# Optimization experiments

Measured on AMD Instinct MI355X. Metric: run time of the kernel, lower is better.

The kernel has to match this reference:

```python
import jax, jax.numpy as jnp
import numpy as np

B, IN_DIM, N, L = 8, 2, 512, 64
D_MODEL = 32
D_FF = 32          # must equal D_MODEL: output_bn is BatchNorm2d(d_model) applied to skip
DEPTH = 3          # blocks=3 * layers=1; dilation resets to 1 each block -> all dilations = 1
KS = 2             # temporal kernel size
EPS = 1e-5         # BatchNorm eps


def setup_inputs() -> dict:
    key = jax.random.key(0)
    ks = jax.random.split(key, 16)
    s = 0.1  # weight scale for numeric sanity
    x = jax.random.normal(ks[0], (B, IN_DIM, N, L), jnp.float32)
    a = jax.random.uniform(ks[1], (N, N), jnp.float32)
    adj = a / a.sum(axis=1, keepdims=True)  # row-stochastic diffusion matrix
    return {
        "x": x,
        "adj": adj,
        "Wstart": jax.random.normal(ks[2], (D_MODEL, IN_DIM), jnp.float32) * s,
        "bstart": jnp.zeros((D_MODEL,), jnp.float32),
        "Wf": jax.random.normal(ks[3], (DEPTH, D_MODEL, D_MODEL, KS), jnp.float32) * s,
        "bf": jnp.zeros((DEPTH, D_MODEL), jnp.float32),
        "Wg": jax.random.normal(ks[4], (DEPTH, D_MODEL, D_MODEL, KS), jnp.float32) * s,
        "bg": jnp.zeros((DEPTH, D_MODEL), jnp.float32),
        "Wskip": jax.random.normal(ks[5], (DEPTH, D_FF, D_MODEL), jnp.float32) * s,
        "bskip": jnp.zeros((DEPTH, D_FF), jnp.float32),
        "Wgc": jax.random.normal(ks[6], (DEPTH, D_MODEL, 3 * D_MODEL), jnp.float32) * s,
        "bgc": jnp.zeros((DEPTH, D_MODEL), jnp.float32),
        "gcbn_g": jnp.ones((DEPTH, D_MODEL), jnp.float32),
        "gcbn_b": jnp.zeros((DEPTH, D_MODEL), jnp.float32),
        "bn_g": jnp.ones((DEPTH, D_MODEL), jnp.float32),
        "bn_b": jnp.zeros((DEPTH, D_MODEL), jnp.float32),
        "obn_g": jnp.ones((D_MODEL,), jnp.float32),
        "obn_b": jnp.zeros((D_MODEL,), jnp.float32),
    }


def _c1x1(x, W, b):
    # Conv2d with (1,1) kernel == channel mixing. x: [b,c,n,l], W: [o,c]
    return jnp.einsum('bcnl,oc->bonl', x, W) + b[None, :, None, None]


def _dconv(x, W, b, d):
    # Conv2d kernel (1,2), dilation d along time (valid). W: [o,c,2]
    Lx = x.shape[-1]
    y = (jnp.einsum('bcnl,oc->bonl', x[..., :Lx - d], W[..., 0])
         + jnp.einsum('bcnl,oc->bonl', x[..., d:], W[..., 1]))
    return y + b[None, :, None, None]


def _bn(x, g, bta):
    # eval-mode BatchNorm2d: running_mean=0, running_var=1
    inv = g / jnp.sqrt(1.0 + EPS)
    return x * inv[None, :, None, None] + bta[None, :, None, None]


def reference(x, adj, Wstart, bstart, Wf, bf, Wg, bg, Wskip, bskip,
              Wgc, bgc, gcbn_g, gcbn_b, bn_g, bn_b, obn_g, obn_b):
    rf = 1 + DEPTH * (KS - 1)  # receptive field with dilation 1 per layer
    h = _c1x1(x, Wstart, bstart)
    if h.shape[-1] < rf:
        h = jnp.pad(h, ((0, 0), (0, 0), (0, 0), (rf - h.shape[-1], 0)))
    skip = None
    for i in range(DEPTH):
        residual = h
        filt = jnp.tanh(_dconv(h, Wf[i], bf[i], 1))
        gate = jax.nn.sigmoid(_dconv(h, Wg[i], bg[i], 1))
        h = filt * gate
        s = _c1x1(h, Wskip[i], bskip[i])
        skip = s if skip is None else s + skip[..., -s.shape[-1]:]
        if i == DEPTH - 1:
            break
        # order-2 graph diffusion: h, A h, A^2 h -> concat -> 1x1 conv -> BN (dropout: eval noop)
        x1 = jnp.einsum('bcnl,nm->bcml', h, adj)
        x2 = jnp.einsum('bcnl,nm->bcml', x1, adj)
        cat = jnp.concatenate([h, x1, x2], axis=1)
        g = _bn(_c1x1(cat, Wgc[i], bgc[i]), gcbn_g[i], gcbn_b[i])
        h = g + residual[..., -g.shape[-1]:]
        h = _bn(h, bn_g[i], bn_b[i])
    out = _bn(skip, obn_g, obn_b)
    return jnp.swapaxes(out, 1, 3)  # [B, L', N, C]
```

## Files before the change

### kernel.cpp

```cpp
#include <hip/hip_runtime.h>
#include <hip/hip_bf16.h>

#define B_     8
#define CIN_   2
#define N_     512
#define C_     32
#define L_     64
#define LOUT_  61
#define BUF_   ((size_t)(8*32*512*64))

typedef __hip_bfloat16 bf16;
typedef unsigned short ushort_t;
typedef unsigned int u32;
typedef __attribute__((ext_vector_type(8))) unsigned short us8;
typedef __attribute__((ext_vector_type(8))) short bf16x8;
typedef __attribute__((ext_vector_type(4))) float f32x4;

static __device__ __forceinline__ float bits2f(ushort_t u) {
    return __uint_as_float(((unsigned)u) << 16);
}
static __device__ __forceinline__ ushort_t f2bits(float v) {
    unsigned u = __float_as_uint(v);
    return (ushort_t)((u + 0x7fffu + ((u >> 16) & 1u)) >> 16);
}

static __device__ __forceinline__ void gload16(const ushort_t* g, ushort_t* l) {
    __builtin_amdgcn_global_load_lds(
        (const __attribute__((address_space(1))) unsigned int*)g,
        (__attribute__((address_space(3))) unsigned int*)l,
        16, 0, 0);
}

static __device__ __forceinline__ u32 swap1(u32 v) {
    return (u32)__builtin_amdgcn_update_dpp(0, (int)v, 0xB1, 0xF, 0xF, true);
}

__global__ void k_start(const float* __restrict__ x,
                        const float* __restrict__ Wst,
                        const float* __restrict__ bst,
                        ushort_t* __restrict__ h) {
    int idx = blockIdx.x * 256 + threadIdx.x;
    int l0 = (idx & 7) * 8;
    int n  = (idx >> 3) & 511;
    int o  = (idx >> 12) & 31;
    int b  = idx >> 17;
    float w0 = Wst[o * 2], w1 = Wst[o * 2 + 1], bb = bst[o];
    int xbase = (b * CIN_ * N_ + n) * L_ + l0;
    float va[8], vb[8];
    *(float4*)&va[0] = *(const float4*)(x + xbase);
    *(float4*)&va[4] = *(const float4*)(x + xbase + 4);
    *(float4*)&vb[0] = *(const float4*)(x + xbase + N_ * L_);
    *(float4*)&vb[4] = *(const float4*)(x + xbase + N_ * L_ + 4);
    us8 r;
    #pragma unroll
    for (int k = 0; k < 8; ++k) r[k] = f2bits(bb + va[k] * w0 + vb[k] * w1);
    *(us8*)(h + (size_t)idx * 8) = r;
}

__global__ void k_transA(const float* __restrict__ adj, ushort_t* __restrict__ adjT) {
    __shared__ float buf[64][65];
    int ti = blockIdx.x & 7;
    int tj = blockIdx.x >> 3;
    int t = threadIdx.x;
    for (int r = 0; r < 16; ++r) {
        int e = t + 256 * r;
        int rl = e >> 6, cl = e & 63;
        buf[rl][cl] = adj[(size_t)(ti * 64 + rl) * 512 + tj * 64 + cl];
    }
    __syncthreads();
    for (int r = 0; r < 16; ++r) {
        int e = t + 256 * r;
        int ml = e >> 6, nl = e & 63;
        adjT[(size_t)(tj * 64 + ml) * 512 + ti * 64 + nl] = f2bits(buf[nl][ml]);
    }
}

__global__ __launch_bounds__(256, 2) void k_sq(const ushort_t* __restrict__ adjT,
                                               ushort_t* __restrict__ adj2T) {
    __shared__ __align__(16) ushort_t lds2[8192];
    ushort_t* As = lds2;
    ushort_t* Bs = lds2 + 4096;
    int mt = blockIdx.x & 7, nc = blockIdx.x >> 3;
    int t = threadIdx.x, lane = t & 63, w = t >> 6;
    int la = lane & 15, q = lane >> 4;
    f32x4 acc[4];
    #pragma unroll
    for (int mi = 0; mi < 4; ++mi) acc[mi] = (f32x4)0.f;
    for (int p0 = 0; p0 < 512; p0 += 64) {
        __syncthreads();
        #pragma unroll
        for (int r = 0; r < 2; ++r) {
            int e = t + 256 * r, ml = e >> 3, oct = e & 7;
            int sw = ((oct + (ml >> 3)) & 7) << 3;
            *(us8*)(As + ml * 64 + sw) =
                *(const us8*)(adjT + (size_t)(mt * 64 + ml) * 512 + p0 + oct * 8);
            *(us8*)(Bs + ml * 64 + sw) =
                *(const us8*)(adjT + (size_t)(p0 + ml) * 512 + nc * 64 + oct * 8);
        }
        __syncthreads();
        #pragma unroll
        for (int ks = 0; ks < 2; ++ks) {
            bf16x8 a[4];
            #pragma unroll
            for (int mi = 0; mi < 4; ++mi) {
                int m = mi * 16 + la;
                int bl = (ks * 4 + q + (m >> 3)) & 7;
                a[mi] = *(const bf16x8*)(As + m * 64 + bl * 8);
            }
            bf16x8 bv;
            {
                int n = w * 16 + la;
                int rot = ((n >> 3) + ks * 4 + q) & 7;
                int col = rot * 8 + (n & 7);
                const ushort_t* p = Bs + (ks * 32 + q * 8) * 64 + col;
                #pragma unroll
                for (int j = 0; j < 8; ++j) bv[j] = (short)p[j * 64];
            }
            #pragma unroll
            for (int mi = 0; mi < 4; ++mi)
                acc[mi] = __builtin_amdgcn_mfma_f32_16x16x32_bf16(a[mi], bv, acc[mi], 0, 0, 0);
        }
    }
    __syncthreads();
    ushort_t* Ys = lds2;
    #pragma unroll
    for (int mi = 0; mi < 4; ++mi)
        #pragma unroll
        for (int r = 0; r < 4; ++r)
            Ys[(mi * 16 + q * 4 + r) * 72 + w * 16 + la] = f2bits(acc[mi][r]);
    __syncthreads();
    #pragma unroll
    for (int r = 0; r < 2; ++r) {
        int e = t + 256 * r, ml = e >> 3, oct = e & 7;
        us8 v = *(const us8*)(Ys + ml * 72 + oct * 8);
        *(us8*)(adj2T + (size_t)(mt * 64 + ml) * 512 + nc * 64 + oct * 8) = v;
    }
}

__global__ __launch_bounds__(256, 6) void k_gs_mfma(
        const ushort_t* __restrict__ h,
        const float* __restrict__ Wf, const float* __restrict__ bfp,
        const float* __restrict__ Wg, const float* __restrict__ bgp,
        const float* __restrict__ Wsk, const float* __restrict__ bsk,
        ushort_t* __restrict__ G, float* __restrict__ out,
        int off, int mode, int storeG,
        const float* __restrict__ og, const float* __restrict__ obb) {
    __shared__ __align__(16) ushort_t lds[10496];
    ushort_t* Hs  = lds;
    ushort_t* Asf = lds + 4608;
    ushort_t* Asg = lds + 6912;
    ushort_t* As2 = lds + 9216;
    __shared__ float bfv[32], bgv[32], bsv[32];
    int t = threadIdx.x;
    int b = blockIdx.x >> 8, n0 = (blockIdx.x & 255) * 2;
    int lane = t & 63, w = t >> 6;
    int ng = w & 1, cg = w >> 1;
    int la = lane & 15, q = lane >> 4;

    {
        int o = t >> 3, k8 = (t & 7) * 8;
        us8 vf, vg;
        #pragma unroll
        for (int i = 0; i < 8; ++i) {
            int k = k8 + i, c = k & 31, tap = k >> 5;
            vf[i] = f2bits(Wf[o * 64 + c * 2 + tap]);
            vg[i] = f2bits(Wg[o * 64 + c * 2 + tap]);
        }
        *(us8*)(Asf + o * 72 + k8) = vf;
        *(us8*)(Asg + o * 72 + k8) = vg;
        if (k8 < 32) {
            us8 vs;
            #pragma unroll
            for (int i = 0; i < 8; ++i) vs[i] = f2bits(Wsk[o * 32 + k8 + i]);
            *(us8*)(As2 + o * 40 + k8) = vs;
        }
        if (t < 32) { bfv[t] = bfp[t]; bgv[t] = bgp[t]; bsv[t] = bsk[t]; }
    }
    const ushort_t* hb = h + (size_t)(b * 32) * 512 * 64;
    #pragma unroll
    for (int r = 0; r < 2; ++r) {
        int e = t + 256 * r;
        int row = e >> 3, oct = e & 7;
        us8 v = *(const us8*)(hb + ((size_t)(row >> 1) * 512 + n0 + (row & 1)) * 64 + oct * 8);
        int sw = (oct + row + (row >> 5)) & 7;
        *(us8*)(Hs + row * 72 + sw * 8) = v;
    }
    if (t < 128) {
        int row = t >> 1, hf = t & 1;
        *(uint2*)(Hs + row * 72 + 64 + hf * 4) = make_uint2(0u, 0u);
    }
    __syncthreads();

    bf16x8 af[2][2], ag[2][2];
    #pragma unroll
    for (int mt = 0; mt < 2; ++mt)
        #pragma unroll
        for (int ks = 0; ks < 2; ++ks) {
            af[mt][ks] = *(const bf16x8*)(Asf + (mt * 16 + la) * 72 + ks * 32 + q * 8);
            ag[mt][ks] = *(const bf16x8*)(Asg + (mt * 16 + la) * 72 + ks * 32 + q * 8);
        }

    f32x4 fa[2][2], ga[2][2];
    #pragma unroll
    for (int mt = 0; mt < 2; ++mt)
        #pragma unroll
        for (int cl = 0; cl < 2; ++cl) { fa[mt][cl] = (f32x4)0.f; ga[mt][cl] = (f32x4)0.f; }
    #pragma unroll
    for (int cl = 0; cl < 2; ++cl) {
        int ct = cg * 2 + cl;
        #pragma unroll
        for (int ks = 0; ks < 2; ++ks) {
            int le = ct * 16 + la + ks;
            bf16x8 bv;
            #pragma unroll
            for (int j = 0; j < 8; ++j) {
                int row = (q * 8 + j) * 2 + ng;
                int pos = (le < 64) ? ((((le >> 3) + row + (row >> 5)) & 7) * 8 + (le & 7)) : le;
                bv[j] = (short)Hs[row * 72 + pos];
            }
            #pragma unroll
            for (int mt = 0; mt < 2; ++mt) {
                fa[mt][cl] = __builtin_amdgcn_mfma_f32_16x16x32_bf16(af[mt][ks], bv, fa[mt][cl], 0, 0, 0);
                ga[mt][cl] = __builtin_amdgcn_mfma_f32_16x16x32_bf16(ag[mt][ks], bv, ga[mt][cl], 0, 0, 0);
            }
        }
    }
    __syncthreads();

    #pragma unroll
    for (int mt = 0; mt < 2; ++mt)
        #pragma unroll
        for (int cl = 0; cl < 2; ++cl)
            #pragma unroll
            for (int r = 0; r < 4; ++r) {
                int o = mt * 16 + q * 4 + r;
                float fv = fa[mt][cl][r] + bfv[o];
                float gv = ga[mt][cl][r] + bgv[o];
                float ef = __expf(2.f * fv);
                float act = (1.f - 2.f / (ef + 1.f)) * (1.f / (1.f + __expf(-gv)));
                int l = (cg * 2 + cl) * 16 + la;
                int row = o * 2 + ng;
                int sw = ((l >> 3) + row + (row >> 5)) & 7;
                Hs[row * 72 + sw * 8 + (l & 7)] = f2bits(act);
            }
    __syncthreads();

    bf16x8 a2[2];
    a2[0] = *(const bf16x8*)(As2 + la * 40 + q * 8);
    a2[1] = *(const bf16x8*)(As2 + (16 + la) * 40 + q * 8);
    f32x4 sa[2][2];
    #pragma unroll
    for (int mt = 0; mt < 2; ++mt)
        #pragma unroll
        for (int cl = 0; cl < 2; ++cl) sa[mt][cl] = (f32x4)0.f;
    #pragma unroll
    for (int cl = 0; cl < 2; ++cl) {
        int le = (cg * 2 + cl) * 16 + la + off;
        bf16x8 bv;
        #pragma unroll
        for (int j = 0; j < 8; ++j) {
            int row = (q * 8 + j) * 2 + ng;
            int pos = (le < 64) ? ((((le >> 3) + row + (row >> 5)) & 7) * 8 + (le & 7)) : le;
            bv[j] = (short)Hs[row * 72 + pos];
        }
        sa[0][cl] = __builtin_amdgcn_mfma_f32_16x16x32_bf16(a2[0], bv, sa[0][cl], 0, 0, 0);
        sa[1][cl] = __builtin_amdgcn_mfma_f32_16x16x32_bf16(a2[1], bv, sa[1][cl], 0, 0, 0);
    }
    __syncthreads();

    if (storeG) {
        #pragma unroll
        for (int r = 0; r < 2; ++r) {
            int e = t + 256 * r;
            int row = e >> 3, oct = e & 7;
            int sw = (oct + row + (row >> 5)) & 7;
            us8 v = *(const us8*)(Hs + row * 72 + sw * 8);
            *(us8*)(G + ((size_t)(b * 32 + (row >> 1)) * 512 + n0 + (row & 1)) * 64 + oct * 8) = v;
        }
    }
    __syncthreads();

    float* St = (float*)lds;
    const float rbn = rsqrtf(1.f + 1e-5f);
    #pragma unroll
    for (int mt = 0; mt < 2; ++mt)
        #pragma unroll
        for (int cl = 0; cl < 2; ++cl) {
            int col = ng * 64 + (cg * 2 + cl) * 16 + la;
            int ob = mt * 16 + q * 4;
            float4 sv = make_float4(sa[mt][cl][0] + bsv[ob],
                                    sa[mt][cl][1] + bsv[ob + 1],
                                    sa[mt][cl][2] + bsv[ob + 2],
                                    sa[mt][cl][3] + bsv[ob + 3]);
            *(float4*)(St + col * 36 + ob) = sv;
        }
    __syncthreads();
    {
        int col = t >> 1, o0 = (t & 1) * 16;
        int nr = col >> 6, l = col & 63;
        if (l < LOUT_) {
            float* po = out + ((size_t)(b * LOUT_ + l) * 512 + n0 + nr) * 32 + o0;
            #pragma unroll
            for (int i = 0; i < 4; ++i) {
                float4 s = *(float4*)(St + col * 36 + o0 + i * 4);
                if (mode == 0) {
                    *(float4*)(po + i * 4) = s;
                } else {
                    float4 old = *(float4*)(po + i * 4);
                    float4 vv = make_float4(old.x + s.x, old.y + s.y,
                                            old.z + s.z, old.w + s.w);
                    if (mode == 2) {
                        int ob = o0 + i * 4;
                        vv.x = vv.x * (og[ob] * rbn) + obb[ob];
                        vv.y = vv.y * (og[ob + 1] * rbn) + obb[ob + 1];
                        vv.z = vv.z * (og[ob + 2] * rbn) + obb[ob + 2];
                        vv.w = vv.w * (og[ob + 3] * rbn) + obb[ob + 3];
                    }
                    *(float4*)(po + i * 4) = vv;
                }
            }
        }
    }
}

__global__ __launch_bounds__(256, 2) void k_diffuse2(
        const ushort_t* __restrict__ X, const ushort_t* __restrict__ adjT,
        const ushort_t* __restrict__ adj2T,
        ushort_t* __restrict__ Y1, ushort_t* __restrict__ Y2) {
    __shared__ __align__(16) ushort_t lds[32768];
    int cp = blockIdx.x & 15;
    int mt = (blockIdx.x >> 4) & 7;
    int b  = blockIdx.x >> 7;
    int t  = threadIdx.x;
    int lane = t & 63, w = t >> 6;
    int c_loc = w & 1, lh = w >> 1;
    int m0 = mt * 64;
    int la = lane & 15, q = lane >> 4;
    int p_ = la & 1;
    u32 sel = p_ ? 0x07060302u : 0x05040100u;
    const ushort_t* Xb = X + (size_t)(b * 32 + cp * 2) * 512 * 64;
    f32x4 acc1[4][2], acc2[4][2];
    #pragma unroll
    for (int mi = 0; mi < 4; ++mi)
        #pragma unroll
        for (int li = 0; li < 2; ++li) { acc1[mi][li] = (f32x4)0.f; acc2[mi][li] = (f32x4)0.f; }

    union U { u32 u[4]; bf16x8 v; };

    auto STAGE = [&](int n0, ushort_t* bb) {
        ushort_t* As1b = bb;
        ushort_t* As2b = bb + 4096;
        ushort_t* Xsb  = bb + 8192;
        #pragma unroll
        for (int r = 0; r < 2; ++r) {
            int e = t + 256 * r, ml = e >> 3, s = e & 7;
            int og = ((s - (ml >> 3)) & 7) * 8;
            gload16(adjT  + (size_t)(m0 + ml) * 512 + n0 + og, As1b + (size_t)e * 8);
            gload16(adj2T + (size_t)(m0 + ml) * 512 + n0 + og, As2b + (size_t)e * 8);
        }
        #pragma unroll
        for (int r = 0; r < 4; ++r) {
            int e = t + 256 * r;
            int cl = e >> 9, nl = (e >> 3) & 63, s = e & 7;
            int og = ((s - nl - (nl >> 3)) & 7) * 8;
            gload16(Xb + ((size_t)cl * 512 + n0 + nl) * 64 + og, Xsb + (size_t)e * 8);
        }
    };

    STAGE(0, lds);
    __syncthreads();

    for (int it = 0; it < 8; ++it) {
        ushort_t* cur = lds + (it & 1) * 16384;
        if (it < 7) STAGE((it + 1) * 64, lds + ((it + 1) & 1) * 16384);
        ushort_t* As1 = cur;
        ushort_t* As2 = cur + 4096;
        ushort_t* Xs  = cur + 8192;
        const ushort_t* xc = Xs + c_loc * 4096;
        #pragma unroll
        for (int ks = 0; ks < 2; ++ks) {
            bf16x8 a1[4], a2v[4];
            #pragma unroll
            for (int mi = 0; mi < 4; ++mi) {
                int m = mi * 16 + la;
                int bl = (ks * 4 + q + (m >> 3)) & 7;
                a1[mi]  = *(const bf16x8*)(As1 + m * 64 + bl * 8);
                a2v[mi] = *(const bf16x8*)(As2 + m * 64 + bl * 8);
            }
            bf16x8 bb[2];
            #pragma unroll
            for (int li = 0; li < 2; ++li) {
                int l2 = lh * 32 + li * 16 + (la & ~1);
                int r0 = ks * 32 + q * 8 + p_ * 4;
                int brot = ((l2 >> 3) + p_ * 4 + ks * 4 + q) & 7;
                u32 o0 = *(const u32*)(xc + (r0 + 0) * 64 + (((brot + 0) & 7) << 3) + (l2 & 7));
                u32 o1 = *(const u32*)(xc + (r0 + 1) * 64 + (((brot + 1) & 7) << 3) + (l2 & 7));
                u32 o2 = *(const u32*)(xc + (r0 + 2) * 64 + (((brot + 2) & 7) << 3) + (l2 & 7));
                u32 o3 = *(const u32*)(xc + (r0 + 3) * 64 + (((brot + 3) & 7) << 3) + (l2 & 7));
                u32 s0 = swap1(o0), s1 = swap1(o1), s2 = swap1(o2), s3 = swap1(o3);
                u32 lo0 = p_ ? s0 : o0, lo1 = p_ ? s1 : o1;
                u32 lo2 = p_ ? s2 : o2, lo3 = p_ ? s3 : o3;
                u32 hi0 = p_ ? o0 : s0, hi1 = p_ ? o1 : s1;
                u32 hi2 = p_ ? o2 : s2, hi3 = p_ ? o3 : s3;
                U u;
                u.u[0] = __builtin_amdgcn_perm(lo1, lo0, sel);
                u.u[1] = __builtin_amdgcn_perm(lo3, lo2, sel);
                u.u[2] = __builtin_amdgcn_perm(hi1, hi0, sel);
                u.u[3] = __builtin_amdgcn_perm(hi3, hi2, sel);
                bb[li] = u.v;
            }
            #pragma unroll
            for (int mi = 0; mi < 4; ++mi)
                #pragma unroll
                for (int li = 0; li < 2; ++li) {
                    acc1[mi][li] = __builtin_amdgcn_mfma_f32_16x16x32_bf16(a1[mi],  bb[li], acc1[mi][li], 0, 0, 0);
                    acc2[mi][li] = __builtin_amdgcn_mfma_f32_16x16x32_bf16(a2v[mi], bb[li], acc2[mi][li], 0, 0, 0);
                }
        }
        __syncthreads();
    }

    ushort_t* Ys = lds;
    #pragma unroll
    for (int pass = 0; pass < 2; ++pass) {
        __syncthreads();
        f32x4 (*src)[2] = pass ? acc2 : acc1;
        #pragma unroll
        for (int mi = 0; mi < 4; ++mi)
            #pragma unroll
            for (int li = 0; li < 2; ++li)
                #pragma unroll
                for (int r = 0; r < 4; ++r) {
                    int row = mi * 16 + q * 4 + r;
                    int col = lh * 32 + li * 16 + la;
                    Ys[c_loc * 4608 + row * 72 + col] = f2bits(src[mi][li][r]);
                }
        __syncthreads();
        ushort_t* Yo = pass ? Y2 : Y1;
        int c = t >> 7, mrem = t & 127;
        int m = mrem >> 1, lq = mrem & 1;
        #pragma unroll
        for (int r = 0; r < 4; ++r) {
            int l0 = lq * 32 + r * 8;
            us8 v = *(const us8*)(Ys + c * 4608 + m * 72 + l0);
            *(us8*)(Yo + ((size_t)(b * 32 + cp * 2 + c) * 512 + m0 + m) * 64 + l0) = v;
        }
    }
}

__global__ __launch_bounds__(256, 2) void k_gc3_mfma(
        ushort_t* __restrict__ G, const ushort_t* __restrict__ X1,
        const ushort_t* __restrict__ X2, const ushort_t* __restrict__ hres,
        const float* __restrict__ Wgc, const float* __restrict__ bgc,
        const float* __restrict__ gg, const float* __restrict__ gb,
        const float* __restrict__ bg2, const float* __restrict__ bb2) {
    __shared__ __align__(16) ushort_t cat[384 * 72];
    __shared__ __align__(16) ushort_t hr[128 * 64];
    __shared__ __align__(16) ushort_t Aw[32 * 104];
    __shared__ float prm[5][32];
    int t = threadIdx.x;
    int b = blockIdx.x >> 7, n0 = (blockIdx.x & 127) * 4;
    int lane = t & 63, w = t >> 6;
    int la = lane & 15, q = lane >> 4;

    #pragma unroll
    for (int r = 0; r < 12; ++r) {
        int e = t + 256 * r;
        int row = e >> 3, oct = e & 7;
        int k = row >> 2;
        const ushort_t* src = (k < 32) ? G : ((k < 64) ? X1 : X2);
        us8 v = *(const us8*)(src + ((size_t)(b * 32 + (k & 31)) * 512 + n0 + (row & 3)) * 64 + oct * 8);
        int sw = (oct + row + (row >> 5)) & 7;
        *(us8*)(cat + row * 72 + sw * 8) = v;
    }
    #pragma unroll
    for (int r = 0; r < 4; ++r) {
        int e = t + 256 * r;
        int row = e >> 3, oct = e & 7;
        us8 v = *(const us8*)(hres + ((size_t)(b * 32 + (row >> 2)) * 512 + n0 + (row & 3)) * 64 + oct * 8);
        *(us8*)(hr + row * 64 + oct * 8) = v;
    }
    for (int e = t; e < 384; e += 256) {
        int o = e / 12, oct = e % 12;
        us8 v;
        #pragma unroll
        for (int i = 0; i < 8; ++i) v[i] = f2bits(Wgc[o * 96 + oct * 8 + i]);
        *(us8*)(Aw + o * 104 + oct * 8) = v;
    }
    if (t < 32) {
        prm[0][t] = bgc[t]; prm[1][t] = gg[t]; prm[2][t] = gb[t];
        prm[3][t] = bg2[t]; prm[4][t] = bb2[t];
    }
    __syncthreads();

    bf16x8 a[2][3];
    #pragma unroll
    for (int mt = 0; mt < 2; ++mt)
        #pragma unroll
        for (int ks = 0; ks < 3; ++ks)
            a[mt][ks] = *(const bf16x8*)(Aw + (mt * 16 + la) * 104 + ks * 32 + q * 8);

    f32x4 acc[2][4];
    #pragma unroll
    for (int mt = 0; mt < 2; ++mt)
        #pragma unroll
        for (int ct = 0; ct < 4; ++ct) acc[mt][ct] = (f32x4)0.f;
    #pragma unroll
    for (int ct = 0; ct < 4; ++ct) {
        int le = ct * 16 + la;
        #pragma unroll
        for (int ks = 0; ks < 3; ++ks) {
            bf16x8 bv;
            #pragma unroll
            for (int j = 0; j < 8; ++j) {
                int row = (ks * 32 + q * 8 + j) * 4 + w;
                int sw = ((le >> 3) + row + (row >> 5)) & 7;
                bv[j] = (short)cat[row * 72 + sw * 8 + (le & 7)];
            }
            acc[0][ct] = __builtin_amdgcn_mfma_f32_16x16x32_bf16(a[0][ks], bv, acc[0][ct], 0, 0, 0);
            acc[1][ct] = __builtin_amdgcn_mfma_f32_16x16x32_bf16(a[1][ks], bv, acc[1][ct], 0, 0, 0);
        }
    }
    __syncthreads();

    const float rbn = rsqrtf(1.f + 1e-5f);
    #pragma unroll
    for (int mt = 0; mt < 2; ++mt)
        #pragma unroll
        for (int ct = 0; ct < 4; ++ct)
            #pragma unroll
            for (int r = 0; r < 4; ++r) {
                int o = mt * 16 + q * 4 + r;
                int l = ct * 16 + la;
                float v = acc[mt][ct][r] + prm[0][o];
                v = v * (prm[1][o] * rbn) + prm[2][o];
                float res = (l < 63) ? bits2f(hr[(o * 4 + w) * 64 + l + 1]) : 0.f;
                v = (v + res) * (prm[3][o] * rbn) + prm[4][o];
                int row = o * 4 + w;
                int sw = ((l >> 3) + row + (row >> 5)) & 7;
                cat[row * 72 + sw * 8 + (l & 7)] = f2bits(v);
            }
    __syncthreads();
    #pragma unroll
    for (int r = 0; r < 4; ++r) {
        int e = t + 256 * r;
        int row = e >> 3, oct = e & 7;
        int sw = (oct + row + (row >> 5)) & 7;
        us8 v = *(const us8*)(cat + row * 72 + sw * 8);
        *(us8*)(G + ((size_t)(b * 32 + (row >> 2)) * 512 + n0 + (row & 3)) * 64 + oct * 8) = v;
    }
}

extern "C" void kernel_launch(void* const* d_in, const int* in_sizes, int n_in,
                              void* d_out, int out_size, void* d_ws, size_t ws_size,
                              hipStream_t stream) {
    const float* x      = (const float*)d_in[0];
    const float* adj    = (const float*)d_in[1];
    const float* Wstart = (const float*)d_in[2];
    const float* bstart = (const float*)d_in[3];
    const float* Wf     = (const float*)d_in[4];
    const float* bf_    = (const float*)d_in[5];
    const float* Wg     = (const float*)d_in[6];
    const float* bg     = (const float*)d_in[7];
    const float* Wskip  = (const float*)d_in[8];
    const float* bskip  = (const float*)d_in[9];
    const float* Wgc    = (const float*)d_in[10];
    const float* bgc    = (const float*)d_in[11];
    const float* gcbn_g = (const float*)d_in[12];
    const float* gcbn_b = (const float*)d_in[13];
    const float* bn_g   = (const float*)d_in[14];
    const float* bn_b   = (const float*)d_in[15];
    const float* obn_g  = (const float*)d_in[16];
    const float* obn_b  = (const float*)d_in[17];
    float* out = (float*)d_out;

    ushort_t* P0    = (ushort_t*)d_ws;
    ushort_t* P1    = P0 + BUF_;
    ushort_t* P2    = P1 + BUF_;
    ushort_t* P3    = P2 + BUF_;
    ushort_t* adjT  = P3 + BUF_;
    ushort_t* adj2T = adjT + 512 * 512;

    k_transA<<<64, 256, 0, stream>>>(adj, adjT);
    k_sq<<<64, 256, 0, stream>>>(adjT, adj2T);
    k_start<<<4096, 256, 0, stream>>>(x, Wstart, bstart, P0);

    ushort_t* h  = P0;
    ushort_t* Gb = P1;
    for (int i = 0; i < 3; ++i) {
        int mode = (i == 0) ? 0 : ((i == 2) ? 2 : 1);
        k_gs_mfma<<<2048, 256, 0, stream>>>(h, Wf + i * 2048, bf_ + i * 32,
                                            Wg + i * 2048, bg + i * 32,
                                            Wskip + i * 1024, bskip + i * 32,
                                            Gb, out, 2 - i, mode, (i < 2) ? 1 : 0,
                                            obn_g, obn_b);
        if (i == 2) break;
        k_diffuse2<<<1024, 256, 0, stream>>>(Gb, adjT, adj2T, P2, P3);
        k_gc3_mfma<<<1024, 256, 0, stream>>>(Gb, P2, P3, h,
                                             Wgc + i * 3072, bgc + i * 32,
                                             gcbn_g + i * 32, gcbn_b + i * 32,
                                             bn_g + i * 32, bn_b + i * 32);
        ushort_t* tmp = h; h = Gb; Gb = tmp;
    }
}
```

Before: 320.7 us.

## Halve gc3 tile to 2 nodes per block and pack B-operand reads

The graph-conv mixing kernel now handles 2 nodes per block instead of 4 and launches twice as many blocks. Its LDS footprint shrinks, the rotated layout drops padding, and the tile is loaded with async gload16 copies. B fragments are built from 32-bit LDS reads combined with byte-perm instructions, replacing per-element 16-bit loads. Launch bounds change for both the gate/skip kernel (fewer waves) and the gc3 kernel (more waves). The swizzle and perm logic is intricate and could introduce layout errors.

New measurement: 306.3 us. 4.5% less time.

```diff
diff --git a/kernel.cpp b/kernel.cpp
--- a/kernel.cpp
+++ b/kernel.cpp
@@ -137,7 +137,7 @@
     }
 }
 
-__global__ __launch_bounds__(256, 6) void k_gs_mfma(
+__global__ __launch_bounds__(256, 4) void k_gs_mfma(
         const ushort_t* __restrict__ h,
         const float* __restrict__ Wf, const float* __restrict__ bfp,
         const float* __restrict__ Wg, const float* __restrict__ bgp,
@@ -448,37 +448,41 @@
     }
 }
 
-__global__ __launch_bounds__(256, 2) void k_gc3_mfma(
+__global__ __launch_bounds__(256, 4) void k_gc3_mfma(
         ushort_t* __restrict__ G, const ushort_t* __restrict__ X1,
         const ushort_t* __restrict__ X2, const ushort_t* __restrict__ hres,
         const float* __restrict__ Wgc, const float* __restrict__ bgc,
         const float* __restrict__ gg, const float* __restrict__ gb,
         const float* __restrict__ bg2, const float* __restrict__ bb2) {
-    __shared__ __align__(16) ushort_t cat[384 * 72];
-    __shared__ __align__(16) ushort_t hr[128 * 64];
+    __shared__ __align__(16) ushort_t cat[192 * 64];
+    __shared__ __align__(16) ushort_t hr[64 * 64];
     __shared__ __align__(16) ushort_t Aw[32 * 104];
     __shared__ float prm[5][32];
     int t = threadIdx.x;
-    int b = blockIdx.x >> 7, n0 = (blockIdx.x & 127) * 4;
+    int b = blockIdx.x >> 8, n0 = (blockIdx.x & 255) * 2;
     int lane = t & 63, w = t >> 6;
+    int ng = w & 1, cg = w >> 1;
     int la = lane & 15, q = lane >> 4;
-
-    #pragma unroll
-    for (int r = 0; r < 12; ++r) {
+    int p_ = la & 1;
+    u32 sel = p_ ? 0x07060302u : 0x05040100u;
+
+    #pragma unroll
+    for (int r = 0; r < 6; ++r) {
+        int e = t + 256 * r;
+        int row = e >> 3, s = e & 7;
+        int k = row >> 1, nr = row & 1;
+        int rot = k + (k >> 3);
+        int og = ((s - rot) & 7) * 8;
+        const ushort_t* src = (k < 32) ? G : ((k < 64) ? X1 : X2);
+        gload16(src + ((size_t)(b * 32 + (k & 31)) * 512 + n0 + nr) * 64 + og,
+                cat + (size_t)e * 8);
+    }
+    #pragma unroll
+    for (int r = 0; r < 2; ++r) {
         int e = t + 256 * r;
         int row = e >> 3, oct = e & 7;
-        int k = row >> 2;
-        const ushort_t* src = (k < 32) ? G : ((k < 64) ? X1 : X2);
-        us8 v = *(const us8*)(src + ((size_t)(b * 32 + (k & 31)) * 512 + n0 + (row & 3)) * 64 + oct * 8);
-        int sw = (oct + row + (row >> 5)) & 7;
-        *(us8*)(cat + row * 72 + sw * 8) = v;
-    }
-    #pragma unroll
-    for (int r = 0; r < 4; ++r) {
-        int e = t + 256 * r;
-        int row = e >> 3, oct = e & 7;
-        us8 v = *(const us8*)(hres + ((size_t)(b * 32 + (row >> 2)) * 512 + n0 + (row & 3)) * 64 + oct * 8);
-        *(us8*)(hr + row * 64 + oct * 8) = v;
+        gload16(hres + ((size_t)(b * 32 + (row >> 1)) * 512 + n0 + (row & 1)) * 64 + oct * 8,
+                hr + (size_t)e * 8);
     }
     for (int e = t; e < 384; e += 256) {
         int o = e / 12, oct = e % 12;
@@ -500,25 +504,35 @@
         for (int ks = 0; ks < 3; ++ks)
             a[mt][ks] = *(const bf16x8*)(Aw + (mt * 16 + la) * 104 + ks * 32 + q * 8);
 
-    f32x4 acc[2][4];
-    #pragma unroll
-    for (int mt = 0; mt < 2; ++mt)
-        #pragma unroll
-        for (int ct = 0; ct < 4; ++ct) acc[mt][ct] = (f32x4)0.f;
-    #pragma unroll
-    for (int ct = 0; ct < 4; ++ct) {
-        int le = ct * 16 + la;
+    union U { u32 u[4]; bf16x8 v; };
+    f32x4 acc[2][2];
+    #pragma unroll
+    for (int mt = 0; mt < 2; ++mt)
+        #pragma unroll
+        for (int cl = 0; cl < 2; ++cl) acc[mt][cl] = (f32x4)0.f;
+    #pragma unroll
+    for (int cl = 0; cl < 2; ++cl) {
+        int l2 = (cg * 2 + cl) * 16 + (la & ~1);
         #pragma unroll
         for (int ks = 0; ks < 3; ++ks) {
-            bf16x8 bv;
-            #pragma unroll
-            for (int j = 0; j < 8; ++j) {
-                int row = (ks * 32 + q * 8 + j) * 4 + w;
-                int sw = ((le >> 3) + row + (row >> 5)) & 7;
-                bv[j] = (short)cat[row * 72 + sw * 8 + (le & 7)];
-            }
-            acc[0][ct] = __builtin_amdgcn_mfma_f32_16x16x32_bf16(a[0][ks], bv, acc[0][ct], 0, 0, 0);
-            acc[1][ct] = __builtin_amdgcn_mfma_f32_16x16x32_bf16(a[1][ks], bv, acc[1][ct], 0, 0, 0);
+            int rb = (ks * 64 + q * 16 + p_ * 8 + ng);
+            int brot = ((l2 >> 3) + p_ * 4 + ks * 4 + q) & 7;
+            u32 o0 = *(const u32*)(cat + (rb + 0) * 64 + (((brot + 0) & 7) << 3) + (l2 & 7));
+            u32 o1 = *(const u32*)(cat + (rb + 2) * 64 + (((brot + 1) & 7) << 3) + (l2 & 7));
+            u32 o2 = *(const u32*)(cat + (rb + 4) * 64 + (((brot + 2) & 7) << 3) + (l2 & 7));
+            u32 o3 = *(const u32*)(cat + (rb + 6) * 64 + (((brot + 3) & 7) << 3) + (l2 & 7));
+            u32 s0 = swap1(o0), s1 = swap1(o1), s2 = swap1(o2), s3 = swap1(o3);
+            u32 lo0 = p_ ? s0 : o0, lo1 = p_ ? s1 : o1;
+            u32 lo2 = p_ ? s2 : o2, lo3 = p_ ? s3 : o3;
+            u32 hi0 = p_ ? o0 : s0, hi1 = p_ ? o1 : s1;
+            u32 hi2 = p_ ? o2 : s2, hi3 = p_ ? o3 : s3;
+            U u;
+            u.u[0] = __builtin_amdgcn_perm(lo1, lo0, sel);
+            u.u[1] = __builtin_amdgcn_perm(lo3, lo2, sel);
+            u.u[2] = __builtin_amdgcn_perm(hi1, hi0, sel);
+            u.u[3] = __builtin_amdgcn_perm(hi3, hi2, sel);
+            acc[0][cl] = __builtin_amdgcn_mfma_f32_16x16x32_bf16(a[0][ks], u.v, acc[0][cl], 0, 0, 0);
+            acc[1][cl] = __builtin_amdgcn_mfma_f32_16x16x32_bf16(a[1][ks], u.v, acc[1][cl], 0, 0, 0);
         }
     }
     __syncthreads();
@@ -527,27 +541,29 @@
     #pragma unroll
     for (int mt = 0; mt < 2; ++mt)
         #pragma unroll
-        for (int ct = 0; ct < 4; ++ct)
+        for (int cl = 0; cl < 2; ++cl)
             #pragma unroll
             for (int r = 0; r < 4; ++r) {
                 int o = mt * 16 + q * 4 + r;
-                int l = ct * 16 + la;
-                float v = acc[mt][ct][r] + prm[0][o];
+                int l = (cg * 2 + cl) * 16 + la;
+                float v = acc[mt][cl][r] + prm[0][o];
                 v = v * (prm[1][o] * rbn) + prm[2][o];
-                float res = (l < 63) ? bits2f(hr[(o * 4 + w) * 64 + l + 1]) : 0.f;
+                float res = (l < 63) ? bits2f(hr[(o * 2 + ng) * 64 + l + 1]) : 0.f;
                 v = (v + res) * (prm[3][o] * rbn) + prm[4][o];
-                int row = o * 4 + w;
-                int sw = ((l >> 3) + row + (row >> 5)) & 7;
-                cat[row * 72 + sw * 8 + (l & 7)] = f2bits(v);
-            }
-    __syncthreads();
-    #pragma unroll
-    for (int r = 0; r < 4; ++r) {
+                int row = o * 2 + ng;
+                int rot = o + (o >> 3);
+                int slot = ((l >> 3) + rot) & 7;
+                cat[row * 64 + slot * 8 + (l & 7)] = f2bits(v);
+            }
+    __syncthreads();
+    #pragma unroll
+    for (int r = 0; r < 2; ++r) {
         int e = t + 256 * r;
-        int row = e >> 3, oct = e & 7;
-        int sw = (oct + row + (row >> 5)) & 7;
-        us8 v = *(const us8*)(cat + row * 72 + sw * 8);
-        *(us8*)(G + ((size_t)(b * 32 + (row >> 2)) * 512 + n0 + (row & 3)) * 64 + oct * 8) = v;
+        int row = e >> 3, og = e & 7;
+        int o = row >> 1, nr = row & 1;
+        int slot = (og + o + (o >> 3)) & 7;
+        us8 v = *(const us8*)(cat + row * 64 + slot * 8);
+        *(us8*)(G + ((size_t)(b * 32 + o) * 512 + n0 + nr) * 64 + og * 8) = v;
     }
 }
 
@@ -596,7 +612,7 @@
                                             obn_g, obn_b);
         if (i == 2) break;
         k_diffuse2<<<1024, 256, 0, stream>>>(Gb, adjT, adj2T, P2, P3);
-        k_gc3_mfma<<<1024, 256, 0, stream>>>(Gb, P2, P3, h,
+        k_gc3_mfma<<<2048, 256, 0, stream>>>(Gb, P2, P3, h,
                                              Wgc + i * 3072, bgc + i * 32,
                                              gcbn_g + i * 32, gcbn_b + i * 32,
                                              bn_g + i * 32, bn_b + i * 32);
```
